# Kernel tuning notes

Measured on AMD Instinct MI355X. Metric: run time of the kernel, lower is better.

The kernel has to match this reference:

```python
import jax, jax.numpy as jnp
import numpy as np

HIDDEN, HEADS, HDIM = 1024, 8, 64
B, S = 4, 8192
LN_EPS = 1e-6


def setup_inputs() -> dict:
    key = jax.random.key(0)
    ks = jax.random.split(key, 12)
    inner = HEADS * HDIM
    sd = HIDDEN ** -0.5
    return {
        "x": jax.random.normal(ks[0], (B, S, HIDDEN), jnp.float32),
        "Wq": jax.random.normal(ks[1], (HIDDEN, inner), jnp.float32) * sd,
        "bq": jnp.zeros((inner,), jnp.float32),
        "Wk": jax.random.normal(ks[2], (HIDDEN, inner), jnp.float32) * sd,
        "bk": jnp.zeros((inner,), jnp.float32),
        "Wv": jax.random.normal(ks[3], (HIDDEN, inner), jnp.float32) * sd,
        "bv": jnp.zeros((inner,), jnp.float32),
        "Wo": jax.random.normal(ks[4], (inner, HIDDEN), jnp.float32) * (inner ** -0.5),
        "bo": jnp.zeros((HIDDEN,), jnp.float32),
        "alpha": jnp.ones((HEADS, HDIM), jnp.float32),
        "aug_param": jax.random.normal(ks[5], (1, HEADS, HDIM), jnp.float32),
        "ln_scale": jnp.ones((HIDDEN,), jnp.float32),
        "ln_bias": jnp.zeros((HIDDEN,), jnp.float32),
    }


def reference(x, Wq, bq, Wk, bk, Wv, bv, Wo, bo, alpha, aug_param, ln_scale, ln_bias):
    b, s, _ = x.shape
    h, d = alpha.shape
    scale = d ** -0.5
    q = (x @ Wq + bq).reshape(b, s, h, d)
    k = (x @ Wk + bk).reshape(b, s, h, d)
    v = (x @ Wv + bv).reshape(b, s, h, d)
    decay = jax.nn.sigmoid(alpha)  # (h, d)

    def step(state, qkv):
        q_t, k_t, v_t = qkv  # each (b, h, d)
        attn = jax.nn.softmax(jnp.einsum('bhd,bhd->bh', q_t, k_t) * scale, axis=-1)
        new_state = decay * state + (1.0 - decay) * attn[..., None] * v_t
        return new_state, new_state

    qs = jnp.moveaxis(q, 1, 0)  # (s, b, h, d)
    ks_ = jnp.moveaxis(k, 1, 0)
    vs = jnp.moveaxis(v, 1, 0)
    init = jnp.zeros((b, h, d), x.dtype)
    _, states = jax.lax.scan(step, init, (qs, ks_, vs))
    states = jnp.moveaxis(states, 0, 1)  # (b, s, h, d)

    aug = jax.nn.sigmoid(q * aug_param)  # aug_param (1,h,d) broadcasts over (b,s,h,d)
    out = (q * states + aug).reshape(b, s, h * d)
    out = out @ Wo + bo
    mean = jnp.mean(out, axis=-1, keepdims=True)
    var = jnp.var(out, axis=-1, keepdims=True)
    return (out - mean) * jax.lax.rsqrt(var + LN_EPS) * ln_scale + ln_bias
```

## Files before the change

kernel.cpp:

```cpp
#include <hip/hip_runtime.h>
#include <hip/hip_bf16.h>


#define HIDDEN 1024
#define HEADS 8
#define HDIM 64
#define INNER 512
#define BATCH 4
#define SEQ 8192
#define ROWS (BATCH*SEQ)
#define NCHUNK 128
#define CHLEN 64

typedef unsigned short u16;
typedef unsigned int u32;
typedef __attribute__((ext_vector_type(8))) short bf16x8;
typedef __attribute__((ext_vector_type(4))) float f32x4;

__device__ __forceinline__ float b2f(u16 u) { return __uint_as_float(((u32)u) << 16); }
__device__ __forceinline__ u16 f2b(float f) {
  u32 u = __float_as_uint(f);
  u32 r = u + 0x7fffu + ((u >> 16) & 1u);
  return (u16)(r >> 16);
}
__device__ __forceinline__ u32 pack2(float a, float b) {
  return (u32)f2b(a) | ((u32)f2b(b) << 16);
}

#define GLOAD_LDS16(gp, lp)                                                  \
  __builtin_amdgcn_global_load_lds(                                          \
      (const __attribute__((address_space(1))) u32*)(gp),                    \
      (__attribute__((address_space(3))) u32*)(lp), 16, 0, 0)

__global__ __launch_bounds__(256) void prep_x(const float* __restrict__ x,
                                              u16* __restrict__ xb) {
  size_t i = ((size_t)blockIdx.x * 256 + threadIdx.x) * 8;
  float4 a = *(const float4*)(x + i);
  float4 b = *(const float4*)(x + i + 4);
  uint4 w = {pack2(a.x, a.y), pack2(a.z, a.w), pack2(b.x, b.y), pack2(b.z, b.w)};
  *(uint4*)(xb + i) = w;
}

__global__ __launch_bounds__(256) void prep_w(
    const float* __restrict__ Wq, const float* __restrict__ Wk,
    const float* __restrict__ Wv, const float* __restrict__ Wo,
    const float* __restrict__ bq, const float* __restrict__ bk,
    const float* __restrict__ bv,
    u16* __restrict__ Wt, u16* __restrict__ Wot, float* __restrict__ bcat) {
  const int WELEM = HIDDEN * INNER;
  int idx = blockIdx.x * 256 + threadIdx.x;
  if (idx < 3 * WELEM) {
    int z = idx / WELEM;
    int rem = idx - z * WELEM;
    int n = rem >> 10;
    int k = rem & 1023;
    const float* W = (z == 0) ? Wq : (z == 1) ? Wk : Wv;
    Wt[idx] = f2b(W[k * INNER + n]);
  } else {
    int rem = idx - 3 * WELEM;
    int n = rem >> 9;
    int k = rem & 511;
    Wot[rem] = f2b(Wo[k * HIDDEN + n]);
  }
  if (idx < 3 * INNER) {
    int z = idx >> 9;
    int n = idx & 511;
    bcat[idx] = (z == 0) ? bq[n] : (z == 1) ? bk[n] : bv[n];
  }
}

template <int K, bool OUT_F32, bool SPLIT3>
__global__ __launch_bounds__(512, 2) void gemm_8ph(
    const u16* __restrict__ A, const u16* __restrict__ Bt,
    const float* __restrict__ bias,
    void* __restrict__ out0, void* __restrict__ out1, void* __restrict__ out2,
    int nTilesN) {
  constexpr int NT = K / 32;
  __shared__ u16 lds[4][16384];

  const int nwg = gridDim.x;
  const int chunk = nwg >> 3;
  const int bid = blockIdx.x;
  const int lin = (bid & 7) * chunk + (bid >> 3);
  const int nt = lin % nTilesN;
  const int mt = lin / nTilesN;
  const int m0 = mt * 256, n0 = nt * 256;
  const int N = nTilesN * 256;

  const int tid = threadIdx.x;
  const int lane = tid & 63;
  const int w = tid >> 6;
  const int wm = w >> 2;
  const int wn = w & 3;
  const int r16 = lane & 15, kq = lane >> 4;

  const int rt = tid >> 2;
  const int cg = (((tid & 3) << 3)) ^ (((rt >> 1) & 3) << 3);
  const u16* Ag = A + (size_t)(m0 + rt) * K + cg;
  const u16* Bg = Bt + (size_t)(n0 + rt) * K + cg;
  const int ldst = w * 512;

#define STAGE_A(slot, kt)                                                     \
  {                                                                           \
    GLOAD_LDS16(Ag + (size_t)(kt) * 32, &lds[slot][ldst]);                    \
    GLOAD_LDS16(Ag + (size_t)(kt) * 32 + (size_t)128 * K,                     \
                &lds[slot][4096 + ldst]);                                     \
  }
#define STAGE_B(slot, kt)                                                     \
  {                                                                           \
    GLOAD_LDS16(Bg + (size_t)(kt) * 32, &lds[slot][8192 + ldst]);             \
    GLOAD_LDS16(Bg + (size_t)(kt) * 32 + (size_t)128 * K,                     \
                &lds[slot][12288 + ldst]);                                    \
  }

  const int xk = (kq << 3) ^ (((r16 >> 1) & 3) << 3);
  const int aO = (wm * 128 + r16) * 32 + xk;
  const int bO = 8192 + (wn * 64 + r16) * 32 + xk;

  f32x4 acc[8][4] = {};
  bf16x8 af[4], bfv[4];

#define PH0(t_, STG)                                                           \
  {                                                                            \
    const u16* sl = &lds[(t_) & 3][0];                                         \
    _Pragma("unroll") for (int i = 0; i < 4; i++)                              \
        af[i] = *(const bf16x8*)&sl[aO + i * 512];                             \
    _Pragma("unroll") for (int j = 0; j < 4; j++)                              \
        bfv[j] = *(const bf16x8*)&sl[bO + j * 512];                            \
    STG;                                                                       \
    __builtin_amdgcn_sched_barrier(0);                                         \
    __builtin_amdgcn_s_barrier();                                              \
    asm volatile("s_waitcnt lgkmcnt(0)" ::: "memory");                         \
    __builtin_amdgcn_sched_barrier(0);                                         \
    __builtin_amdgcn_s_setprio(1);                                             \
    _Pragma("unroll") for (int i = 0; i < 4; i++)                              \
        _Pragma("unroll") for (int j = 0; j < 4; j++)                          \
            acc[i][j] =                                                        \
        __builtin_amdgcn_mfma_f32_16x16x32_bf16(af[i], bfv[j], acc[i][j], 0, 0, 0); \
    __builtin_amdgcn_s_setprio(0);                                             \
    __builtin_amdgcn_sched_barrier(0);                                         \
    __builtin_amdgcn_s_barrier();                                              \
  }

#define PH1(t_, STG, VM)                                                       \
  {                                                                            \
    const u16* sl = &lds[(t_) & 3][0];                                         \
    _Pragma("unroll") for (int i = 0; i < 4; i++)                              \
        af[i] = *(const bf16x8*)&sl[aO + (i + 4) * 512];                       \
    STG;                                                                       \
    asm volatile("s_waitcnt vmcnt(" #VM ")" ::: "memory");                     \
    __builtin_amdgcn_sched_barrier(0);                                         \
    __builtin_amdgcn_s_barrier();                                              \
    asm volatile("s_waitcnt lgkmcnt(0)" ::: "memory");                         \
    __builtin_amdgcn_sched_barrier(0);                                         \
    __builtin_amdgcn_s_setprio(1);                                             \
    _Pragma("unroll") for (int i = 0; i < 4; i++)                              \
        _Pragma("unroll") for (int j = 0; j < 4; j++)                          \
            acc[i + 4][j] =                                                    \
        __builtin_amdgcn_mfma_f32_16x16x32_bf16(af[i], bfv[j], acc[i + 4][j], 0, 0, 0); \
    __builtin_amdgcn_s_setprio(0);                                             \
    __builtin_amdgcn_sched_barrier(0);                                         \
    __builtin_amdgcn_s_barrier();                                              \
  }

#define NOSTG ((void)0)

  STAGE_A(0, 0); STAGE_B(0, 0);
  STAGE_A(1, 1); STAGE_B(1, 1);
  STAGE_A(2, 2); STAGE_B(2, 2);
  asm volatile("s_waitcnt vmcnt(8)" ::: "memory");
  __builtin_amdgcn_sched_barrier(0);
  __builtin_amdgcn_s_barrier();

  for (int t = 0; t < NT - 3; ++t) {
    PH0(t, STAGE_A((t + 3) & 3, t + 3));
    PH1(t, STAGE_B((t + 3) & 3, t + 3), 8);
  }
  PH0(NT - 3, NOSTG);
  PH1(NT - 3, NOSTG, 4);
  PH0(NT - 2, NOSTG);
  PH1(NT - 2, NOSTG, 0);
  PH0(NT - 1, NOSTG);
  PH1(NT - 1, NOSTG, 0);
#undef PH0
#undef PH1
#undef NOSTG
#undef STAGE_A
#undef STAGE_B

  const int zsel = SPLIT3 ? ((n0 + wn * 64) >> 9) : 0;
  u16* ob16 = (u16*)((zsel == 0) ? out0 : (zsel == 1) ? out1 : out2);
#pragma unroll
  for (int j = 0; j < 4; j++) {
    int col = n0 + wn * 64 + j * 16 + r16;
    float bv = bias[col];
    int colm = SPLIT3 ? (col & 511) : col;
#pragma unroll
    for (int i = 0; i < 8; i++) {
#pragma unroll
      for (int q = 0; q < 4; q++) {
        int row = m0 + wm * 128 + i * 16 + kq * 4 + q;
        float v = acc[i][j][q] + bv;
        if (OUT_F32)
          ((float*)out0)[(size_t)row * N + col] = v;
        else
          ob16[(size_t)row * INNER + colm] = f2b(v);
      }
    }
  }
}

template <bool A_BF16, bool OUT_F32>
__global__ __launch_bounds__(256) void gemm128(
    const void* __restrict__ Aany, const u16* __restrict__ BtBase,
    const float* __restrict__ bias0, const float* __restrict__ bias1,
    const float* __restrict__ bias2,
    void* __restrict__ out0, void* __restrict__ out1, void* __restrict__ out2,
    int K) {
  __shared__ u16 As[128 * 32];
  __shared__ u16 Bs[128 * 32];
  const int N = gridDim.x * 128;
  const int z = blockIdx.z;
  const u16* Bt = BtBase + (size_t)z * N * K;
  const float* bias = (z == 0) ? bias0 : (z == 1) ? bias1 : bias2;
  void* Out = (z == 0) ? out0 : (z == 1) ? out1 : out2;
  const int tid = threadIdx.x;
  const int m0 = blockIdx.y * 128;
  const int n0 = blockIdx.x * 128;
  const int lane = tid & 63;
  const int wid = tid >> 6;
  const int wm = wid >> 1, wn = wid & 1;
  const int r16 = lane & 15, kq = lane >> 4;
  const int r = tid >> 1;
  const int half = tid & 1;
  f32x4 acc[4][4] = {};
  for (int k0 = 0; k0 < K; k0 += 32) {
    __syncthreads();
    if (A_BF16) {
      const u16* Ab = (const u16*)Aany;
      const int4* src = (const int4*)(Ab + (size_t)(m0 + r) * K + k0 + half * 16);
      int4 v0 = src[0];
      int4 v1 = src[1];
      *(int4*)&As[r * 32 + half * 16] = v0;
      *(int4*)&As[r * 32 + half * 16 + 8] = v1;
    } else {
      const float* Af = (const float*)Aany;
      const float4* src = (const float4*)(Af + (size_t)(m0 + r) * K + k0 + half * 16);
      float4 f0 = src[0], f1 = src[1], f2 = src[2], f3 = src[3];
      uint4 w0 = {pack2(f0.x, f0.y), pack2(f0.z, f0.w), pack2(f1.x, f1.y), pack2(f1.z, f1.w)};
      uint4 w1 = {pack2(f2.x, f2.y), pack2(f2.z, f2.w), pack2(f3.x, f3.y), pack2(f3.z, f3.w)};
      *(uint4*)&As[r * 32 + half * 16] = w0;
      *(uint4*)&As[r * 32 + half * 16 + 8] = w1;
    }
    {
      const int4* src = (const int4*)(Bt + (size_t)(n0 + r) * K + k0 + half * 16);
      int4 v0 = src[0];
      int4 v1 = src[1];
      *(int4*)&Bs[r * 32 + half * 16] = v0;
      *(int4*)&Bs[r * 32 + half * 16 + 8] = v1;
    }
    __syncthreads();
    bf16x8 a[4], b[4];
#pragma unroll
    for (int i = 0; i < 4; i++)
      a[i] = *(const bf16x8*)&As[(wm * 64 + i * 16 + r16) * 32 + kq * 8];
#pragma unroll
    for (int j = 0; j < 4; j++)
      b[j] = *(const bf16x8*)&Bs[(wn * 64 + j * 16 + r16) * 32 + kq * 8];
#pragma unroll
    for (int i = 0; i < 4; i++)
#pragma unroll
      for (int j = 0; j < 4; j++)
        acc[i][j] = __builtin_amdgcn_mfma_f32_16x16x32_bf16(a[i], b[j], acc[i][j], 0, 0, 0);
  }
#pragma unroll
  for (int j = 0; j < 4; j++) {
    int col = n0 + wn * 64 + j * 16 + r16;
    float bv = bias[col];
#pragma unroll
    for (int i = 0; i < 4; i++) {
#pragma unroll
      for (int q = 0; q < 4; q++) {
        int row = m0 + wm * 64 + i * 16 + kq * 4 + q;
        float v = acc[i][j][q] + bv;
        if (OUT_F32)
          ((float*)Out)[(size_t)row * N + col] = v;
        else
          ((u16*)Out)[(size_t)row * N + col] = f2b(v);
      }
    }
  }
}

__global__ __launch_bounds__(256) void attn_kernel(
    const u16* __restrict__ qb, const u16* __restrict__ kb,
    float* __restrict__ attn) {
  int lane = threadIdx.x & 63;
  int wid = threadIdx.x >> 6;
  size_t t = (size_t)blockIdx.x * 4 + wid;
  int4 qv = *(const int4*)(qb + t * INNER + lane * 8);
  int4 kv = *(const int4*)(kb + t * INNER + lane * 8);
  const u16* qu = (const u16*)&qv;
  const u16* ku = (const u16*)&kv;
  float s = 0.f;
#pragma unroll
  for (int j = 0; j < 8; j++) s += b2f(qu[j]) * b2f(ku[j]);
  s += __shfl_xor(s, 1);
  s += __shfl_xor(s, 2);
  s += __shfl_xor(s, 4);
  s *= 0.125f;
  float mx = s;
  mx = fmaxf(mx, __shfl_xor(mx, 8));
  mx = fmaxf(mx, __shfl_xor(mx, 16));
  mx = fmaxf(mx, __shfl_xor(mx, 32));
  float e = __expf(s - mx);
  float sm = e;
  sm += __shfl_xor(sm, 8);
  sm += __shfl_xor(sm, 16);
  sm += __shfl_xor(sm, 32);
  float a = e / sm;
  if ((lane & 7) == 0) attn[t * HEADS + (lane >> 3)] = a;
}

__global__ __launch_bounds__(512) void scan_phase1(
    const u16* __restrict__ vb, const float* __restrict__ attn,
    const float* __restrict__ alpha, float* __restrict__ ends) {
  int hd = threadIdx.x;
  int h = hd >> 6;
  int c = blockIdx.x, b = blockIdx.y;
  float decay = 1.f / (1.f + __expf(-alpha[hd]));
  float om = 1.f - decay;
  size_t base = (size_t)b * SEQ + (size_t)c * CHLEN;
  float st = 0.f;
#pragma unroll 8
  for (int i = 0; i < CHLEN; i++) {
    size_t t = base + i;
    float a = attn[t * HEADS + h];
    float v = b2f(vb[t * INNER + hd]);
    st = decay * st + om * a * v;
  }
  ends[((size_t)b * NCHUNK + c) * INNER + hd] = st;
}

__global__ __launch_bounds__(512) void scan_phase2(
    const float* __restrict__ ends, const float* __restrict__ alpha,
    float* __restrict__ carries) {
  int hd = threadIdx.x;
  int b = blockIdx.x;
  float decay = 1.f / (1.f + __expf(-alpha[hd]));
  float dL = __powf(decay, (float)CHLEN);
  float carry = 0.f;
#pragma unroll 8
  for (int c = 0; c < NCHUNK; c++) {
    size_t idx = ((size_t)b * NCHUNK + c) * INNER + hd;
    carries[idx] = carry;
    carry = dL * carry + ends[idx];
  }
}

__global__ __launch_bounds__(512) void scan_phase3(
    const u16* __restrict__ qb, const u16* __restrict__ vb,
    const float* __restrict__ attn, const float* __restrict__ alpha,
    const float* __restrict__ augp, const float* __restrict__ carries,
    u16* __restrict__ outpre) {
  int hd = threadIdx.x;
  int h = hd >> 6;
  int c = blockIdx.x, b = blockIdx.y;
  float decay = 1.f / (1.f + __expf(-alpha[hd]));
  float om = 1.f - decay;
  float ap = augp[hd];
  float st = carries[((size_t)b * NCHUNK + c) * INNER + hd];
  size_t base = (size_t)b * SEQ + (size_t)c * CHLEN;
#pragma unroll 4
  for (int i = 0; i < CHLEN; i++) {
    size_t t = base + i;
    float a = attn[t * HEADS + h];
    float v = b2f(vb[t * INNER + hd]);
    st = decay * st + om * a * v;
    float q = b2f(qb[t * INNER + hd]);
    float aug = 1.f / (1.f + __expf(-q * ap));
    outpre[t * INNER + hd] = f2b(q * st + aug);
  }
}

__global__ __launch_bounds__(256) void ln_kernel(
    float* __restrict__ out, const float* __restrict__ lns,
    const float* __restrict__ lnb) {
  size_t row = blockIdx.x;
  int tid = threadIdx.x;
  float4 v = *(float4*)(out + row * HIDDEN + tid * 4);
  float s = v.x + v.y + v.z + v.w;
  float ss = v.x * v.x + v.y * v.y + v.z * v.z + v.w * v.w;
#pragma unroll
  for (int m = 1; m < 64; m <<= 1) {
    s += __shfl_xor(s, m);
    ss += __shfl_xor(ss, m);
  }
  __shared__ float sb[4], ssb[4];
  int lane = tid & 63, wid = tid >> 6;
  if (lane == 0) {
    sb[wid] = s;
    ssb[wid] = ss;
  }
  __syncthreads();
  s = sb[0] + sb[1] + sb[2] + sb[3];
  ss = ssb[0] + ssb[1] + ssb[2] + ssb[3];
  float mean = s * (1.f / HIDDEN);
  float var = ss * (1.f / HIDDEN) - mean * mean;
  float rstd = rsqrtf(var + 1e-6f);
  float4 sc = *(const float4*)(lns + tid * 4);
  float4 bi = *(const float4*)(lnb + tid * 4);
  v.x = (v.x - mean) * rstd * sc.x + bi.x;
  v.y = (v.y - mean) * rstd * sc.y + bi.y;
  v.z = (v.z - mean) * rstd * sc.z + bi.z;
  v.w = (v.w - mean) * rstd * sc.w + bi.w;
  *(float4*)(out + row * HIDDEN + tid * 4) = v;
}

extern "C" void kernel_launch(void* const* d_in, const int* in_sizes, int n_in,
                              void* d_out, int out_size, void* d_ws, size_t ws_size,
                              hipStream_t stream) {
  const float* x = (const float*)d_in[0];
  const float* Wq = (const float*)d_in[1];
  const float* bq = (const float*)d_in[2];
  const float* Wk = (const float*)d_in[3];
  const float* bk = (const float*)d_in[4];
  const float* Wv = (const float*)d_in[5];
  const float* bv = (const float*)d_in[6];
  const float* Wo = (const float*)d_in[7];
  const float* bo = (const float*)d_in[8];
  const float* alpha = (const float*)d_in[9];
  const float* augp = (const float*)d_in[10];
  const float* lns = (const float*)d_in[11];
  const float* lnb = (const float*)d_in[12];

  char* ws = (char*)d_ws;
  const bool fast = ws_size >= 175118336ull;

  if (fast) {
    u16* xb = (u16*)(ws + 0);
    u16* qb = (u16*)(ws + 67108864);
    u16* kb = (u16*)(ws + 100663296);
    u16* vb = (u16*)(ws + 134217728);
    u16* Wt = (u16*)(ws + 167772160);
    u16* Wot = (u16*)(ws + 170917888);
    float* bcat = (float*)(ws + 171966464);
    float* attn = (float*)(ws + 171972608);
    float* ends = (float*)(ws + 173021184);
    float* car = (float*)(ws + 174069760);
    u16* outpre = kb;

    prep_x<<<ROWS * HIDDEN / 8 / 256, 256, 0, stream>>>(x, xb);
    prep_w<<<8192, 256, 0, stream>>>(Wq, Wk, Wv, Wo, bq, bk, bv, Wt, Wot, bcat);

    gemm_8ph<HIDDEN, false, true><<<768, 512, 0, stream>>>(
        xb, Wt, bcat, qb, kb, vb, 6);

    attn_kernel<<<ROWS / 4, 256, 0, stream>>>(qb, kb, attn);
    scan_phase1<<<dim3(NCHUNK, BATCH), 512, 0, stream>>>(vb, attn, alpha, ends);
    scan_phase2<<<BATCH, 512, 0, stream>>>(ends, alpha, car);
    scan_phase3<<<dim3(NCHUNK, BATCH), 512, 0, stream>>>(qb, vb, attn, alpha, augp, car, outpre);

    gemm_8ph<INNER, true, false><<<512, 512, 0, stream>>>(
        outpre, Wot, bo, d_out, d_out, d_out, 4);

    ln_kernel<<<ROWS, 256, 0, stream>>>((float*)d_out, lns, lnb);
  } else {
    u16* qb = (u16*)(ws + 0);
    u16* kb = (u16*)(ws + 33554432);
    u16* vb = (u16*)(ws + 67108864);
    u16* Wt = (u16*)(ws + 100663296);
    u16* Wot = (u16*)(ws + 103809024);
    float* bcat = (float*)(ws + 104845312);
    float* attn = (float*)(ws + 104857600);
    float* ends = (float*)(ws + 105906176);
    float* car = (float*)(ws + 106954752);
    u16* outpre = kb;

    prep_w<<<8192, 256, 0, stream>>>(Wq, Wk, Wv, Wo, bq, bk, bv, Wt, Wot, bcat);
    gemm128<false, false><<<dim3(4, 256, 3), 256, 0, stream>>>(
        x, Wt, bq, bk, bv, qb, kb, vb, HIDDEN);
    attn_kernel<<<ROWS / 4, 256, 0, stream>>>(qb, kb, attn);
    scan_phase1<<<dim3(NCHUNK, BATCH), 512, 0, stream>>>(vb, attn, alpha, ends);
    scan_phase2<<<BATCH, 512, 0, stream>>>(ends, alpha, car);
    scan_phase3<<<dim3(NCHUNK, BATCH), 512, 0, stream>>>(qb, vb, attn, alpha, augp, car, outpre);
    gemm_8ph<INNER, true, false><<<512, 512, 0, stream>>>(
        outpre, Wot, bo, d_out, d_out, d_out, 4);
    ln_kernel<<<ROWS, 256, 0, stream>>>((float*)d_out, lns, lnb);
  }
}
```

Before: 320.3 us.

## Store GEMM outputs as bf16 via LDS-staged coalesced writes; LN reads bf16

The GEMM epilogue now stages accumulator tiles through shared memory and writes 16-byte packed bf16 rows instead of scattered scalar stores. The output projection now writes a bf16 intermediate into a scratch buffer rather than fp32 into the final output. The layernorm kernel then reads that bf16 buffer and writes fp32. This halves GEMM-output and LN-read traffic and coalesces the stores, at the cost of rounding pre-LN values to bf16.

```diff
diff --git a/kernel.cpp b/kernel.cpp
--- a/kernel.cpp
+++ b/kernel.cpp
@@ -69,7 +69,7 @@
   }
 }
 
-template <int K, bool OUT_F32, bool SPLIT3>
+template <int K, bool SPLIT3>
 __global__ __launch_bounds__(512, 2) void gemm_8ph(
     const u16* __restrict__ A, const u16* __restrict__ Bt,
     const float* __restrict__ bias,
@@ -188,29 +188,44 @@
 #undef STAGE_A
 #undef STAGE_B
 
+  float* fl = (float*)(&lds[0][0]) + w * 4096;
   const int zsel = SPLIT3 ? ((n0 + wn * 64) >> 9) : 0;
-  u16* ob16 = (u16*)((zsel == 0) ? out0 : (zsel == 1) ? out1 : out2);
-#pragma unroll
-  for (int j = 0; j < 4; j++) {
-    int col = n0 + wn * 64 + j * 16 + r16;
-    float bv = bias[col];
-    int colm = SPLIT3 ? (col & 511) : col;
-#pragma unroll
-    for (int i = 0; i < 8; i++) {
-#pragma unroll
-      for (int q = 0; q < 4; q++) {
-        int row = m0 + wm * 128 + i * 16 + kq * 4 + q;
-        float v = acc[i][j][q] + bv;
-        if (OUT_F32)
-          ((float*)out0)[(size_t)row * N + col] = v;
-        else
-          ob16[(size_t)row * INNER + colm] = f2b(v);
+  u16* ob = SPLIT3 ? (u16*)((zsel == 0) ? out0 : (zsel == 1) ? out1 : out2)
+                   : (u16*)out0;
+  const int OC = SPLIT3 ? INNER : N;
+  const int colloc = (lane & 7) * 8;
+  const int gcol = (SPLIT3 ? ((n0 + wn * 64) & 511) : (n0 + wn * 64)) + colloc;
+  const int lrowr = lane >> 3;
+  float bvj[4];
+#pragma unroll
+  for (int j = 0; j < 4; j++) bvj[j] = bias[n0 + wn * 64 + j * 16 + r16];
+
+#pragma unroll
+  for (int pass = 0; pass < 4; ++pass) {
+#pragma unroll
+    for (int ii = 0; ii < 2; ++ii) {
+#pragma unroll
+      for (int j = 0; j < 4; ++j) {
+#pragma unroll
+        for (int q = 0; q < 4; ++q)
+          fl[(ii * 16 + kq * 4 + q) * 68 + j * 16 + r16] =
+              acc[pass * 2 + ii][j][q] + bvj[j];
       }
     }
-  }
-}
-
-template <bool A_BF16, bool OUT_F32>
+#pragma unroll
+    for (int inst = 0; inst < 4; ++inst) {
+      int lr = inst * 8 + lrowr;
+      float4 f0 = *(float4*)&fl[lr * 68 + colloc];
+      float4 f1 = *(float4*)&fl[lr * 68 + colloc + 4];
+      uint4 wv = {pack2(f0.x, f0.y), pack2(f0.z, f0.w),
+                  pack2(f1.x, f1.y), pack2(f1.z, f1.w)};
+      size_t grow = (size_t)(m0 + wm * 128 + pass * 32 + lr);
+      *(uint4*)&ob[grow * OC + gcol] = wv;
+    }
+  }
+}
+
+template <bool A_BF16>
 __global__ __launch_bounds__(256) void gemm128(
     const void* __restrict__ Aany, const u16* __restrict__ BtBase,
     const float* __restrict__ bias0, const float* __restrict__ bias1,
@@ -283,10 +298,7 @@
       for (int q = 0; q < 4; q++) {
         int row = m0 + wm * 64 + i * 16 + kq * 4 + q;
         float v = acc[i][j][q] + bv;
-        if (OUT_F32)
-          ((float*)Out)[(size_t)row * N + col] = v;
-        else
-          ((u16*)Out)[(size_t)row * N + col] = f2b(v);
+        ((u16*)Out)[(size_t)row * N + col] = f2b(v);
       }
     }
   }
@@ -384,13 +396,15 @@
 }
 
 __global__ __launch_bounds__(256) void ln_kernel(
-    float* __restrict__ out, const float* __restrict__ lns,
-    const float* __restrict__ lnb) {
+    const u16* __restrict__ outln, float* __restrict__ out,
+    const float* __restrict__ lns, const float* __restrict__ lnb) {
   size_t row = blockIdx.x;
   int tid = threadIdx.x;
-  float4 v = *(float4*)(out + row * HIDDEN + tid * 4);
-  float s = v.x + v.y + v.z + v.w;
-  float ss = v.x * v.x + v.y * v.y + v.z * v.z + v.w * v.w;
+  uint2 rv = *(const uint2*)(outln + row * HIDDEN + tid * 4);
+  const u16* p = (const u16*)&rv;
+  float v0 = b2f(p[0]), v1 = b2f(p[1]), v2 = b2f(p[2]), v3 = b2f(p[3]);
+  float s = v0 + v1 + v2 + v3;
+  float ss = v0 * v0 + v1 * v1 + v2 * v2 + v3 * v3;
 #pragma unroll
   for (int m = 1; m < 64; m <<= 1) {
     s += __shfl_xor(s, m);
@@ -410,11 +424,12 @@
   float rstd = rsqrtf(var + 1e-6f);
   float4 sc = *(const float4*)(lns + tid * 4);
   float4 bi = *(const float4*)(lnb + tid * 4);
-  v.x = (v.x - mean) * rstd * sc.x + bi.x;
-  v.y = (v.y - mean) * rstd * sc.y + bi.y;
-  v.z = (v.z - mean) * rstd * sc.z + bi.z;
-  v.w = (v.w - mean) * rstd * sc.w + bi.w;
-  *(float4*)(out + row * HIDDEN + tid * 4) = v;
+  float4 o;
+  o.x = (v0 - mean) * rstd * sc.x + bi.x;
+  o.y = (v1 - mean) * rstd * sc.y + bi.y;
+  o.z = (v2 - mean) * rstd * sc.z + bi.z;
+  o.w = (v3 - mean) * rstd * sc.w + bi.w;
+  *(float4*)(out + row * HIDDEN + tid * 4) = o;
 }
 
 extern "C" void kernel_launch(void* const* d_in, const int* in_sizes, int n_in,
@@ -449,11 +464,12 @@
     float* ends = (float*)(ws + 173021184);
     float* car = (float*)(ws + 174069760);
     u16* outpre = kb;
+    u16* outln = xb;
 
     prep_x<<<ROWS * HIDDEN / 8 / 256, 256, 0, stream>>>(x, xb);
     prep_w<<<8192, 256, 0, stream>>>(Wq, Wk, Wv, Wo, bq, bk, bv, Wt, Wot, bcat);
 
-    gemm_8ph<HIDDEN, false, true><<<768, 512, 0, stream>>>(
+    gemm_8ph<HIDDEN, true><<<768, 512, 0, stream>>>(
         xb, Wt, bcat, qb, kb, vb, 6);
 
     attn_kernel<<<ROWS / 4, 256, 0, stream>>>(qb, kb, attn);
@@ -461,14 +477,14 @@
     scan_phase2<<<BATCH, 512, 0, stream>>>(ends, alpha, car);
     scan_phase3<<<dim3(NCHUNK, BATCH), 512, 0, stream>>>(qb, vb, attn, alpha, augp, car, outpre);
 
-    gemm_8ph<INNER, true, false><<<512, 512, 0, stream>>>(
-        outpre, Wot, bo, d_out, d_out, d_out, 4);
-
-    ln_kernel<<<ROWS, 256, 0, stream>>>((float*)d_out, lns, lnb);
+    gemm_8ph<INNER, false><<<512, 512, 0, stream>>>(
+        outpre, Wot, bo, outln, outln, outln, 4);
+
+    ln_kernel<<<ROWS, 256, 0, stream>>>(outln, (float*)d_out, lns, lnb);
   } else {
     u16* qb = (u16*)(ws + 0);
-    u16* kb = (u16*)(ws + 33554432);
-    u16* vb = (u16*)(ws + 67108864);
+    u16* vb = (u16*)(ws + 33554432);
+    u16* kb = (u16*)(ws + 67108864);
     u16* Wt = (u16*)(ws + 100663296);
     u16* Wot = (u16*)(ws + 103809024);
     float* bcat = (float*)(ws + 104845312);
@@ -476,16 +492,17 @@
     float* ends = (float*)(ws + 105906176);
     float* car = (float*)(ws + 106954752);
     u16* outpre = kb;
+    u16* outln = (u16*)(ws + 0);
 
     prep_w<<<8192, 256, 0, stream>>>(Wq, Wk, Wv, Wo, bq, bk, bv, Wt, Wot, bcat);
-    gemm128<false, false><<<dim3(4, 256, 3), 256, 0, stream>>>(
+    gemm128<false><<<dim3(4, 256, 3), 256, 0, stream>>>(
         x, Wt, bq, bk, bv, qb, kb, vb, HIDDEN);
     attn_kernel<<<ROWS / 4, 256, 0, stream>>>(qb, kb, attn);
     scan_phase1<<<dim3(NCHUNK, BATCH), 512, 0, stream>>>(vb, attn, alpha, ends);
     scan_phase2<<<BATCH, 512, 0, stream>>>(ends, alpha, car);
     scan_phase3<<<dim3(NCHUNK, BATCH), 512, 0, stream>>>(qb, vb, attn, alpha, augp, car, outpre);
-    gemm_8ph<INNER, true, false><<<512, 512, 0, stream>>>(
-        outpre, Wot, bo, d_out, d_out, d_out, 4);
-    ln_kernel<<<ROWS, 256, 0, stream>>>((float*)d_out, lns, lnb);
-  }
-}
+    gemm_8ph<INNER, false><<<512, 512, 0, stream>>>(
+        outpre, Wot, bo, outln, outln, outln, 4);
+    ln_kernel<<<ROWS, 256, 0, stream>>>(outln, (float*)d_out, lns, lnb);
+  }
+}
```

Result: faster. 278.8 us (-13.0%).
